# Kernel optimization log

Hardware: AMD Instinct MI355X
Metric: run time of the kernel (lower is better)

The kernel has to match this reference:

```python
import jax, jax.numpy as jnp
import numpy as np

N_QUBITS = 6
N_LAYERS = 2
QSVT_DEGREE = 3
BATCH = 128
SEQ_LEN = 512
DIM = 2 ** N_QUBITS
# wire 0 is the most-significant bit in the statevector index (PennyLane convention)
_POP = np.array([bin(i).count('1') for i in range(DIM)], dtype=np.float32)
PHASE_SIGN = jnp.asarray(N_QUBITS - 2.0 * _POP)  # (DIM,): sum_w (1 - 2*bit_w)


def _rx(t):
    c = jnp.cos(0.5 * t).astype(jnp.complex64)
    s = (-1j * jnp.sin(0.5 * t)).astype(jnp.complex64)
    return jnp.stack([jnp.stack([c, s]), jnp.stack([s, c])])


def _ry(t):
    c = jnp.cos(0.5 * t).astype(jnp.complex64)
    s = jnp.sin(0.5 * t).astype(jnp.complex64)
    return jnp.stack([jnp.stack([c, -s]), jnp.stack([s, c])])


def _rz(t):
    e = jnp.exp(-0.5j * t.astype(jnp.complex64))
    z = jnp.zeros((), jnp.complex64)
    return jnp.stack([jnp.stack([e, z]), jnp.stack([z, jnp.conj(e)])])


def _apply_1q(psi, U, w):
    # psi: (B,) + (2,)*N_QUBITS ; U: (2,2) complex, same for all batch elems
    psi = jnp.moveaxis(psi, 1 + w, -1)
    psi = psi @ U.T
    return jnp.moveaxis(psi, -1, 1 + w)


def _apply_ry_batched(psi, theta, w):
    # RY with a per-batch angle theta: (B,)
    psi = jnp.moveaxis(psi, 1 + w, -1)
    c = jnp.cos(0.5 * theta).reshape((-1,) + (1,) * (N_QUBITS - 1))
    s = jnp.sin(0.5 * theta).reshape((-1,) + (1,) * (N_QUBITS - 1))
    a, b = psi[..., 0], psi[..., 1]
    psi = jnp.stack([c * a - s * b, s * a + c * b], axis=-1)
    return jnp.moveaxis(psi, -1, 1 + w)


def _cnot(psi, c, t):
    p0 = jax.lax.index_in_dim(psi, 0, axis=1 + c, keepdims=True)
    p1 = jax.lax.index_in_dim(psi, 1, axis=1 + c, keepdims=True)
    p1 = jnp.flip(p1, axis=1 + t)
    return jnp.concatenate([p0, p1], axis=1 + c)


def _circuit_step(h, x, params, poly):
    # h, x: (B, N_QUBITS) angles. Returns <Z_w> per qubit: (B, N_QUBITS).
    B = h.shape[0]
    # 1) state encoding: RY(h_w)|0> = cos(h/2)|0> + sin(h/2)|1>  (product state)
    c, s = jnp.cos(0.5 * h), jnp.sin(0.5 * h)
    psi = jnp.ones((B, 1), jnp.complex64)
    for w in range(N_QUBITS):
        amp = jnp.stack([c[:, w], s[:, w]], axis=-1).astype(jnp.complex64)  # (B,2)
        psi = (psi[:, :, None] * amp[:, None, :]).reshape(B, -1)
    psi = psi.reshape((B,) + (2,) * N_QUBITS)
    # 2) QSVT block: RZ(coeff*pi) on every wire fuses into one diagonal phase
    for d in range(QSVT_DEGREE + 1):
        theta = poly[d] * np.pi
        phase = jnp.exp((-0.5j) * theta * PHASE_SIGN)  # (DIM,)
        psi = (psi.reshape(B, -1) * phase[None, :]).reshape((B,) + (2,) * N_QUBITS)
        for i in range(N_QUBITS - 1):
            psi = _cnot(psi, i, i + 1)
        psi = _cnot(psi, N_QUBITS - 1, 0)  # ring closure
    # 3) variational layers: per-wire RZ@RY@RX (RX applied first), then CNOT chain
    idx = 0
    for _ in range(N_LAYERS):
        for i in range(N_QUBITS):
            U = _rz(params[idx + 2]) @ _ry(params[idx + 1]) @ _rx(params[idx])
            psi = _apply_1q(psi, U, i)
            idx += 3
        for i in range(N_QUBITS - 1):
            psi = _cnot(psi, i, i + 1)
    # 4) input injection: RY(x_w) with per-batch angles
    for w in range(N_QUBITS):
        psi = _apply_ry_batched(psi, x[:, w], w)
    # 5) measurement: <Z_w> = P(bit_w=0) - P(bit_w=1)
    p = jnp.abs(psi) ** 2
    zs = []
    for w in range(N_QUBITS):
        axes = tuple(a for a in range(1, N_QUBITS + 1) if a != 1 + w)
        pw = p.sum(axis=axes)  # (B,2)
        zs.append(pw[:, 0] - pw[:, 1])
    return jnp.stack(zs, axis=-1)


def _ssm_pass(angles, params, poly, reverse):
    a = jnp.flip(angles, axis=1) if reverse else angles
    xs = jnp.moveaxis(a, 1, 0)  # (T, B, n)
    h0 = jnp.zeros((a.shape[0], N_QUBITS), jnp.float32)

    def step(h, x):
        hn = _circuit_step(h, x, params, poly)
        return hn, hn

    _, ys = jax.lax.scan(step, h0, xs)
    out = jnp.moveaxis(ys, 0, 1)  # (B, T, n)
    return jnp.flip(out, axis=1) if reverse else out


def setup_inputs() -> dict:
    key = jax.random.key(0)
    k0, k1, k2, k3 = jax.random.split(key, 4)
    angles = jax.random.uniform(k0, (BATCH, SEQ_LEN, N_QUBITS), jnp.float32) * np.float32(np.pi)
    poly_coeffs = jax.random.normal(k1, (QSVT_DEGREE + 1,), jnp.float32) * 0.1
    fwd_params = jax.random.normal(k2, (N_QUBITS * N_LAYERS * 3,), jnp.float32) * 0.1
    bwd_params = jax.random.normal(k3, (N_QUBITS * N_LAYERS * 3,), jnp.float32) * 0.1
    fwd_coeff = jnp.full((1,), 0.5, jnp.float32)
    bwd_coeff = jnp.full((1,), 0.5, jnp.float32)
    return {'angles': angles, 'poly_coeffs': poly_coeffs, 'fwd_params': fwd_params,
            'bwd_params': bwd_params, 'fwd_coeff': fwd_coeff, 'bwd_coeff': bwd_coeff}


def reference(angles, poly_coeffs, fwd_params, bwd_params, fwd_coeff, bwd_coeff):
    h_fwd = _ssm_pass(angles, fwd_params, poly_coeffs, reverse=False)
    h_bwd = _ssm_pass(angles, bwd_params, poly_coeffs, reverse=True)
    return jax.nn.sigmoid(fwd_coeff) * h_fwd + jax.nn.sigmoid(bwd_coeff) * h_bwd
```

## Files before the change

kernel.cpp:

```cpp
#include <hip/hip_runtime.h>
#include <hip/hip_bf16.h>
#include <stdint.h>

#define BATCH 128
#define SEQ   512
#define NW    6
#define DIM   64
#define NELEM (BATCH * SEQ * NW)
#define PI_F  3.14159265358979323846f
#define MSTRIDE 132

typedef float v2f __attribute__((ext_vector_type(2)));

template <int CTRL>
__device__ __forceinline__ void red_stage6(float v[6]) {
#pragma unroll
    for (int w = 0; w < 6; ++w)
        v[w] += __int_as_float(__builtin_amdgcn_update_dpp(
            0, __float_as_int(v[w]), CTRL, 0xF, 0xF, false));
}

__device__ __forceinline__ void sincos_half(float h, float& s, float& c) {
    const float u = h * h;
    c = fmaf(u, fmaf(u, fmaf(u, -2.1701389e-5f, 2.6041667e-3f), -0.125f), 1.0f);
    s = h * fmaf(u, fmaf(u, fmaf(u, -1.5501e-6f, 2.6041667e-4f), -2.0833333e-2f), 0.5f);
}

__global__ void k_detect(const uint32_t* __restrict__ a, int* __restrict__ flag) {
    __shared__ int cnt;
    if (threadIdx.x == 0) cnt = 0;
    __syncthreads();
    uint32_t w = a[threadIdx.x];
    uint32_t e = (w >> 8) & 0xFFu;
    if (e >= 0x3Au && e <= 0x41u) atomicAdd(&cnt, 1);
    __syncthreads();
    if (threadIdx.x == 0) *flag = (cnt >= 128) ? 1 : 0;
}

__device__ __forceinline__ float ldf(const void* p, int i, bool bf) {
    if (bf) {
        uint32_t u = (uint32_t)((const uint16_t*)p)[i];
        return __uint_as_float(u << 16);
    }
    return ((const float*)p)[i];
}

__global__ void k_convert(const void* ang, const void* poly, const void* fp,
                          const void* bp, const void* fc, const void* bc,
                          float* __restrict__ cs, float* __restrict__ misc,
                          const int* __restrict__ flag) {
    const bool bf = (*flag != 0);
    const int i = blockIdx.x * blockDim.x + threadIdx.x;
    if (i < NELEM) {
        float x = ldf(ang, i, bf);
        float s, c;
        __sincosf(x, &s, &c);
        cs[2 * i]     = c;
        cs[2 * i + 1] = s;
    }
    if (i < 4)                    misc[i]            = ldf(poly, i, bf);
    else if (i >= 64 && i < 100)  misc[4 + (i - 64)] = ldf(fp, i - 64, bf);
    else if (i >= 128 && i < 164) misc[40 + (i - 128)] = ldf(bp, i - 128, bf);
    else if (i == 200)            misc[76] = ldf(fc, 0, bf);
    else if (i == 201)            misc[77] = ldf(bc, 0, bf);
}

__global__ void __launch_bounds__(64) k_msetup(const float* __restrict__ misc,
                                               float* __restrict__ Mg) {
    const int p   = threadIdx.x;
    const int col = blockIdx.x & 63;
    const int dir = blockIdx.x >> 6;
    const float* poly = misc;
    const float* prm  = misc + (dir ? 40 : 4);

    float yr = (p == col) ? 1.f : 0.f;
    float yi = 0.f;

#pragma unroll
    for (int d = 0; d < 4; ++d) {
        const float th = 0.5f * PI_F * poly[d] *
                         (float)(6 - 2 * (int)__popc((unsigned)p));
        float s, c;
        __sincosf(th, &s, &c);
        const float nr = yr * c + yi * s;
        const float ni = yi * c - yr * s;
        yr = nr; yi = ni;
#pragma unroll
        for (int k = 0; k < 6; ++k) {
            const int cw = k, tw = (k + 1) % 6;
            const int src = p ^ (((p >> (5 - cw)) & 1) << (5 - tw));
            yr = __shfl(yr, src, 64);
            yi = __shfl(yi, src, 64);
        }
    }

    int idx = 0;
#pragma unroll
    for (int l = 0; l < 2; ++l) {
#pragma unroll
        for (int w = 0; w < 6; ++w) {
            float cx, sx, cy, sy, cz, sz;
            __sincosf(0.5f * prm[idx + 0], &sx, &cx);
            __sincosf(0.5f * prm[idx + 1], &sy, &cy);
            __sincosf(0.5f * prm[idx + 2], &sz, &cz);
            idx += 3;
            const float A = cy * cx, B = sy * sx, C = sy * cx, D = cy * sx;
            const float U00r = cz * A + sz * B, U00i = cz * B - sz * A;
            const float U11r = U00r,            U11i = sz * A - cz * B;
            const float Xr   = cz * C + sz * D, Xi   = sz * C - cz * D;
            const int m  = 1 << (5 - w);
            const int bb = (p >> (5 - w)) & 1;
            const float C1r = bb ? U11r : U00r;
            const float C1i = bb ? U11i : U00i;
            const float C2r = bb ? Xr : -Xr;
            const float C2i = Xi;
            const float pr = __shfl_xor(yr, m, 64);
            const float pi = __shfl_xor(yi, m, 64);
            const float nr = C1r * yr - C1i * yi + C2r * pr - C2i * pi;
            const float ni = C1r * yi + C1i * yr + C2r * pi + C2i * pr;
            yr = nr; yi = ni;
        }
#pragma unroll
        for (int k = 0; k < 5; ++k) {
            const int src = p ^ (((p >> (5 - k)) & 1) << (5 - (k + 1)));
            yr = __shfl(yr, src, 64);
            yi = __shfl(yi, src, 64);
        }
    }

    float* out = Mg + ((size_t)(dir * 64 + p) * 64 + (size_t)col) * 2;
    out[0] = yr;
    out[1] = yi;
}

__global__ void __launch_bounds__(64, 1) k_sim(const float* __restrict__ cs,
                                               const float* __restrict__ Mg,
                                               float* __restrict__ hbuf) {
    const int lane  = threadIdx.x;
    const int chain = blockIdx.x;
    const int dir   = chain >> 7;
    const int b     = chain & 127;
    float* orow = hbuf + (size_t)dir * NELEM + (size_t)b * (SEQ * NW);
    const float* csrow = cs + (size_t)b * (SEQ * NW * 2);

    __shared__ float Ml[DIM * MSTRIDE];
    __shared__ float zb[SEQ * NW];

    {
        const float4* mrow = (const float4*)(Mg + (size_t)(dir * 64 + lane) * 128);
        float4* dst = (float4*)(Ml + lane * MSTRIDE);
#pragma unroll
        for (int cc = 0; cc < 32; ++cc) dst[cc] = mrow[cc];
    }
    __syncthreads();

    int zmask[6];
#pragma unroll
    for (int w = 0; w < 6; ++w) zmask[w] = ((lane >> (5 - w)) & 1) << 31;

    float h[6] = {0.f, 0.f, 0.f, 0.f, 0.f, 0.f};

    const int tin0 = dir ? SEQ - 1 : 0;
    const float4* x0p = (const float4*)(csrow + tin0 * 12);
    float4 xq0 = x0p[0], xq1 = x0p[1], xq2 = x0p[2];

    const float4* Mrow4 = (const float4*)(Ml + lane * MSTRIDE);

    for (int t = 0; t < SEQ; ++t) {
        const int tin  = dir ? (SEQ - 1 - t) : t;
        const int tn   = (t + 1 < SEQ) ? t + 1 : t;
        const int tinn = dir ? (SEQ - 1 - tn) : tn;
        const float4* xnp = (const float4*)(csrow + tinn * 12);
        float4 nx0 = xnp[0], nx1 = xnp[1], nx2 = xnp[2];

        float cw6[6], sw6[6];
#pragma unroll
        for (int w = 0; w < 6; ++w) sincos_half(h[w], sw6[w], cw6[w]);
        float G[8], L[8];
        {
            const float g00 = cw6[0] * cw6[1], g01 = cw6[0] * sw6[1];
            const float g10 = sw6[0] * cw6[1], g11 = sw6[0] * sw6[1];
            G[0] = g00 * cw6[2]; G[1] = g00 * sw6[2];
            G[2] = g01 * cw6[2]; G[3] = g01 * sw6[2];
            G[4] = g10 * cw6[2]; G[5] = g10 * sw6[2];
            G[6] = g11 * cw6[2]; G[7] = g11 * sw6[2];
            const float l00 = cw6[3] * cw6[4], l01 = cw6[3] * sw6[4];
            const float l10 = sw6[3] * cw6[4], l11 = sw6[3] * sw6[4];
            L[0] = l00 * cw6[5]; L[1] = l00 * sw6[5];
            L[2] = l01 * cw6[5]; L[3] = l01 * sw6[5];
            L[4] = l10 * cw6[5]; L[5] = l10 * sw6[5];
            L[6] = l11 * cw6[5]; L[7] = l11 * sw6[5];
        }

        v2f y = {0.f, 0.f};
#pragma unroll
        for (int a = 0; a < 8; ++a) {
            const float4 c0 = Mrow4[4 * a + 0];
            const float4 c1 = Mrow4[4 * a + 1];
            const float4 c2 = Mrow4[4 * a + 2];
            const float4 c3 = Mrow4[4 * a + 3];
            v2f T = {0.f, 0.f};
            T += L[0] * (v2f){c0.x, c0.y};
            T += L[1] * (v2f){c0.z, c0.w};
            T += L[2] * (v2f){c1.x, c1.y};
            T += L[3] * (v2f){c1.z, c1.w};
            T += L[4] * (v2f){c2.x, c2.y};
            T += L[5] * (v2f){c2.z, c2.w};
            T += L[6] * (v2f){c3.x, c3.y};
            T += L[7] * (v2f){c3.z, c3.w};
            y += G[a] * T;
        }
        const float yr = y.x, yi = y.y;

        float pr[6], pi[6];
#pragma unroll
        for (int w = 0; w < 6; ++w) pr[w] = __shfl_xor(yr, 1 << (5 - w), 64);
#pragma unroll
        for (int w = 0; w < 6; ++w) pi[w] = __shfl_xor(yi, 1 << (5 - w), 64);

        const float q = yr * yr + yi * yi;
        float cxw[6], sxw[6];
        cxw[0] = xq0.x; sxw[0] = xq0.y; cxw[1] = xq0.z; sxw[1] = xq0.w;
        cxw[2] = xq1.x; sxw[2] = xq1.y; cxw[3] = xq1.z; sxw[3] = xq1.w;
        cxw[4] = xq2.x; sxw[4] = xq2.y; cxw[5] = xq2.z; sxw[5] = xq2.w;

        float v[6];
#pragma unroll
        for (int w = 0; w < 6; ++w) {
            const float ac = yr * pr[w] + yi * pi[w];
            const float sq = __int_as_float(__float_as_int(q) ^ zmask[w]);
            v[w] = cxw[w] * sq - sxw[w] * ac;
        }

        red_stage6<0x111>(v);
        red_stage6<0x112>(v);
        red_stage6<0x114>(v);
        red_stage6<0x118>(v);
        red_stage6<0x142>(v);
        red_stage6<0x143>(v);

        if (lane == 63) {
#pragma unroll
            for (int w = 0; w < 6; ++w) zb[tin * NW + w] = v[w];
        }

#pragma unroll
        for (int w = 0; w < 6; ++w)
            h[w] = __int_as_float(
                __builtin_amdgcn_readlane(__float_as_int(v[w]), 63));

        xq0 = nx0; xq1 = nx1; xq2 = nx2;
    }
    __syncthreads();

    {
        const float4* zs4 = (const float4*)zb;
        float4* go = (float4*)orow;
#pragma unroll
        for (int k = 0; k < 12; ++k) {
            const int idx = lane + k * 64;
            go[idx] = zs4[idx];
        }
    }
}

__global__ void k_combine(const float* __restrict__ hbuf,
                          const float* __restrict__ misc,
                          void* __restrict__ out, const int* __restrict__ flag) {
    const int i = blockIdx.x * blockDim.x + threadIdx.x;
    if (i >= NELEM) return;
    const float sf = 1.f / (1.f + __expf(-misc[76]));
    const float sb = 1.f / (1.f + __expf(-misc[77]));
    const float v = sf * hbuf[i] + sb * hbuf[NELEM + i];
    if (*flag) ((__hip_bfloat16*)out)[i] = __float2bfloat16(v);
    else       ((float*)out)[i] = v;
}

extern "C" void kernel_launch(void* const* d_in, const int* in_sizes, int n_in,
                              void* d_out, int out_size, void* d_ws, size_t ws_size,
                              hipStream_t stream) {
    const void* ang  = d_in[0];
    const void* poly = d_in[1];
    const void* fp   = d_in[2];
    const void* bp   = d_in[3];
    const void* fc   = d_in[4];
    const void* bc   = d_in[5];

    float* cs   = (float*)d_ws;
    float* misc = cs + 2 * NELEM;
    float* hbuf = misc + 128;
    float* Mg   = hbuf + 2 * NELEM;
    int*   flag = (int*)(Mg + 2 * 64 * 64 * 2);

    k_detect<<<1, 256, 0, stream>>>((const uint32_t*)ang, flag);
    k_convert<<<(NELEM + 255) / 256, 256, 0, stream>>>(ang, poly, fp, bp, fc, bc,
                                                       cs, misc, flag);
    k_msetup<<<128, 64, 0, stream>>>(misc, Mg);
    k_sim<<<256, 64, 0, stream>>>(cs, Mg, hbuf);
    k_combine<<<(NELEM + 255) / 256, 256, 0, stream>>>(hbuf, misc, d_out, flag);
}
```

Baseline: 428.8 us.

## Keep part of M in registers, use packed FMA, bpermute, unroll time loop

```diff
diff --git a/kernel.cpp b/kernel.cpp
--- a/kernel.cpp
+++ b/kernel.cpp
@@ -8,9 +8,13 @@
 #define DIM   64
 #define NELEM (BATCH * SEQ * NW)
 #define PI_F  3.14159265358979323846f
-#define MSTRIDE 132
+#define MSTRIDE 100
 
 typedef float v2f __attribute__((ext_vector_type(2)));
+
+__device__ __forceinline__ v2f pkfma(float s, v2f m, v2f a) {
+    return __builtin_elementwise_fma((v2f){s, s}, m, a);
+}
 
 template <int CTRL>
 __device__ __forceinline__ void red_stage6(float v[6]) {
@@ -147,31 +151,41 @@
     __shared__ float zb[SEQ * NW];
 
     {
-        const float4* mrow = (const float4*)(Mg + (size_t)(dir * 64 + lane) * 128);
+        const float4* mrow =
+            (const float4*)(Mg + (size_t)(dir * 64 + lane) * 128 + 32);
         float4* dst = (float4*)(Ml + lane * MSTRIDE);
 #pragma unroll
-        for (int cc = 0; cc < 32; ++cc) dst[cc] = mrow[cc];
+        for (int k = 0; k < 24; ++k) dst[k] = mrow[k];
+    }
+    v2f Mres[16];
+    {
+        const float2* mr2 = (const float2*)(Mg + (size_t)(dir * 64 + lane) * 128);
+#pragma unroll
+        for (int k = 0; k < 16; ++k) Mres[k] = (v2f){mr2[k].x, mr2[k].y};
     }
     __syncthreads();
 
-    int zmask[6];
-#pragma unroll
-    for (int w = 0; w < 6; ++w) zmask[w] = ((lane >> (5 - w)) & 1) << 31;
+    int zmask[6], bpa[6];
+#pragma unroll
+    for (int w = 0; w < 6; ++w) {
+        zmask[w] = ((lane >> (5 - w)) & 1) << 31;
+        bpa[w]   = (lane ^ (1 << (5 - w))) << 2;
+    }
 
     float h[6] = {0.f, 0.f, 0.f, 0.f, 0.f, 0.f};
 
-    const int tin0 = dir ? SEQ - 1 : 0;
-    const float4* x0p = (const float4*)(csrow + tin0 * 12);
-    float4 xq0 = x0p[0], xq1 = x0p[1], xq2 = x0p[2];
-
     const float4* Mrow4 = (const float4*)(Ml + lane * MSTRIDE);
 
-    for (int t = 0; t < SEQ; ++t) {
-        const int tin  = dir ? (SEQ - 1 - t) : t;
-        const int tn   = (t + 1 < SEQ) ? t + 1 : t;
-        const int tinn = dir ? (SEQ - 1 - tn) : tn;
-        const float4* xnp = (const float4*)(csrow + tinn * 12);
-        float4 nx0 = xnp[0], nx1 = xnp[1], nx2 = xnp[2];
+    const float* cp = csrow + (dir ? (SEQ - 1) * 12 : 0);
+    const int   cstep = dir ? -12 : 12;
+    float*       zp = zb + (dir ? (SEQ - 1) * NW : 0);
+    const int   zstep = dir ? -NW : NW;
+
+    auto step = [&](const float4 xq0, const float4 xq1, const float4 xq2,
+                    float* zout) {
+        float4 mb[24];
+#pragma unroll
+        for (int k = 0; k < 24; ++k) mb[k] = Mrow4[k];
 
         float cw6[6], sw6[6];
 #pragma unroll
@@ -194,29 +208,38 @@
 
         v2f y = {0.f, 0.f};
 #pragma unroll
-        for (int a = 0; a < 8; ++a) {
-            const float4 c0 = Mrow4[4 * a + 0];
-            const float4 c1 = Mrow4[4 * a + 1];
-            const float4 c2 = Mrow4[4 * a + 2];
-            const float4 c3 = Mrow4[4 * a + 3];
+        for (int a = 0; a < 2; ++a) {
             v2f T = {0.f, 0.f};
-            T += L[0] * (v2f){c0.x, c0.y};
-            T += L[1] * (v2f){c0.z, c0.w};
-            T += L[2] * (v2f){c1.x, c1.y};
-            T += L[3] * (v2f){c1.z, c1.w};
-            T += L[4] * (v2f){c2.x, c2.y};
-            T += L[5] * (v2f){c2.z, c2.w};
-            T += L[6] * (v2f){c3.x, c3.y};
-            T += L[7] * (v2f){c3.z, c3.w};
-            y += G[a] * T;
+#pragma unroll
+            for (int bb2 = 0; bb2 < 8; ++bb2)
+                T = pkfma(L[bb2], Mres[8 * a + bb2], T);
+            y = pkfma(G[a], T, y);
+        }
+#pragma unroll
+        for (int a = 2; a < 8; ++a) {
+            const int o = 4 * a - 8;
+            v2f T = {0.f, 0.f};
+            T = pkfma(L[0], (v2f){mb[o + 0].x, mb[o + 0].y}, T);
+            T = pkfma(L[1], (v2f){mb[o + 0].z, mb[o + 0].w}, T);
+            T = pkfma(L[2], (v2f){mb[o + 1].x, mb[o + 1].y}, T);
+            T = pkfma(L[3], (v2f){mb[o + 1].z, mb[o + 1].w}, T);
+            T = pkfma(L[4], (v2f){mb[o + 2].x, mb[o + 2].y}, T);
+            T = pkfma(L[5], (v2f){mb[o + 2].z, mb[o + 2].w}, T);
+            T = pkfma(L[6], (v2f){mb[o + 3].x, mb[o + 3].y}, T);
+            T = pkfma(L[7], (v2f){mb[o + 3].z, mb[o + 3].w}, T);
+            y = pkfma(G[a], T, y);
         }
         const float yr = y.x, yi = y.y;
 
         float pr[6], pi[6];
 #pragma unroll
-        for (int w = 0; w < 6; ++w) pr[w] = __shfl_xor(yr, 1 << (5 - w), 64);
-#pragma unroll
-        for (int w = 0; w < 6; ++w) pi[w] = __shfl_xor(yi, 1 << (5 - w), 64);
+        for (int w = 0; w < 6; ++w)
+            pr[w] = __int_as_float(
+                __builtin_amdgcn_ds_bpermute(bpa[w], __float_as_int(yr)));
+#pragma unroll
+        for (int w = 0; w < 6; ++w)
+            pi[w] = __int_as_float(
+                __builtin_amdgcn_ds_bpermute(bpa[w], __float_as_int(yi)));
 
         const float q = yr * yr + yi * yi;
         float cxw[6], sxw[6];
@@ -241,15 +264,35 @@
 
         if (lane == 63) {
 #pragma unroll
-            for (int w = 0; w < 6; ++w) zb[tin * NW + w] = v[w];
-        }
-
+            for (int w = 0; w < 6; ++w) zout[w] = v[w];
+        }
 #pragma unroll
         for (int w = 0; w < 6; ++w)
             h[w] = __int_as_float(
                 __builtin_amdgcn_readlane(__float_as_int(v[w]), 63));
-
-        xq0 = nx0; xq1 = nx1; xq2 = nx2;
+    };
+
+    float4 xa0 = ((const float4*)cp)[0];
+    float4 xa1 = ((const float4*)cp)[1];
+    float4 xa2 = ((const float4*)cp)[2];
+
+    for (int t = 0; t < SEQ; t += 2) {
+        const float* cp1 = cp + cstep;
+        const float4 xb0 = ((const float4*)cp1)[0];
+        const float4 xb1 = ((const float4*)cp1)[1];
+        const float4 xb2 = ((const float4*)cp1)[2];
+
+        step(xa0, xa1, xa2, zp);
+        zp += zstep;
+
+        const float* cp2 = cp + 2 * cstep;
+        xa0 = ((const float4*)cp2)[0];
+        xa1 = ((const float4*)cp2)[1];
+        xa2 = ((const float4*)cp2)[2];
+
+        step(xb0, xb1, xb2, zp);
+        zp += zstep;
+        cp = cp2;
     }
     __syncthreads();
 
@@ -286,7 +329,7 @@
     const void* fc   = d_in[4];
     const void* bc   = d_in[5];
 
-    float* cs   = (float*)d_ws;
+    float* cs   = (float*)d_ws + 32;
     float* misc = cs + 2 * NELEM;
     float* hbuf = misc + 128;
     float* Mg   = hbuf + 2 * NELEM;
```

New measurement: 444.1 us. 1.04x slower.
